# Kernel optimization log

Measured on AMD Instinct MI355X. Metric: run time of the kernel, lower is better.

The kernel has to match this reference:

```python
import jax, jax.numpy as jnp
import numpy as np

N, D, C, S = 100000, 512, 4096, 50000


def setup_inputs() -> dict:
    key = jax.random.key(0)
    k1, k2 = jax.random.split(key)
    X = jax.random.normal(k1, (N, D), dtype=jnp.float32)
    codebook_sum = jax.random.normal(k2, (C, D), dtype=jnp.float32)
    prompt_mask = jnp.arange(N) < S  # first S rows are support (True), rest are queries
    return {"X": X, "codebook_sum": codebook_sum, "prompt_mask": prompt_mask, "num_support": S}


def reference(X, codebook_sum, prompt_mask, num_support):
    # num_support is a static Python int (replaces torch.nonzero(prompt_mask) dynamic split)
    s = num_support
    support = X[:s]                                   # [S, D] support (prompt_mask==True)
    query = X[s:]                                     # [Q, D] queries (prompt_mask==False)
    # dense similarity matmul + top-1 nearest-codebook search + gather
    cos_sim = jnp.einsum('sd,cd->sc', support, codebook_sum)  # [S, C]
    top_idx = jnp.argmax(cos_sim, axis=1)             # [S]
    code_n = codebook_sum[top_idx]                    # [S, D] gathered nearest codes
    # mean-pooled prototypes broadcast over queries
    proto = jnp.mean(support, axis=0)                 # [D]
    proto_code = jnp.mean(code_n, axis=0)             # [D]
    # euclidean distances to each prototype
    query_score = jnp.sqrt(jnp.sum((query - proto) ** 2, axis=1))        # [Q]
    query_score_code = jnp.sqrt(jnp.sum((query - proto_code) ** 2, axis=1))  # [Q]
    return (query_score + query_score_code) / 2
```

## Files before the change

kernel.cpp:

```cpp
#include <hip/hip_runtime.h>
#include <hip/hip_bf16.h>

#define NTOT 100000
#define DIM  512
#define CB   4096
#define SSUP 50000
#define NQ   (NTOT - SSUP)

#define MTILES 391
#define MPAD   (MTILES * 128)
#define NTILES 32
#define NBLOCKS (MTILES * NTILES)

typedef __bf16 bf16x8 __attribute__((ext_vector_type(8)));
typedef __bf16 bf16x4 __attribute__((ext_vector_type(4)));
typedef float  f32x4  __attribute__((ext_vector_type(4)));
typedef float  f32x16 __attribute__((ext_vector_type(16)));

#define OFF_CBBF   0
#define OFF_XB     4194304
#define OFF_PV     55443456
#define OFF_PI     61849600
#define OFF_PSUM   68255744
#define OFF_PCSUM  68257792
#define OFF_HIST   68259840
#define WS_NEED    (68259840 + 16384)
#define ZERO_BYTES (2048 + 2048 + 16384)

#define F_OFF_PSUM   4194304
#define F_OFF_PCSUM  4196352
#define F_OFF_HIST   4198400
#define F_OFF_TIDX   4214784

__device__ __forceinline__ void load_lds16(const void* g, void* l) {
    __builtin_amdgcn_global_load_lds(
        (const __attribute__((address_space(1))) void*)g,
        (__attribute__((address_space(3))) void*)l, 16, 0, 0);
}

__global__ void k_convert(const float* __restrict__ src, __bf16* __restrict__ dst) {
    int i = (blockIdx.x * 256 + threadIdx.x) * 4;
    float4 v = *(const float4*)(src + i);
    bf16x4 o;
    o[0] = (__bf16)v.x; o[1] = (__bf16)v.y; o[2] = (__bf16)v.z; o[3] = (__bf16)v.w;
    *(bf16x4*)(dst + i) = o;
}

__global__ void k_prep_support(const float* __restrict__ X, __bf16* __restrict__ Xb,
                               float* __restrict__ protoSum) {
    const int tid   = threadIdx.x;
    const int rhalf = tid >> 7;
    const int c4    = (tid & 127) * 4;
    const size_t r0 = (size_t)blockIdx.x * 128;
    float a0 = 0.f, a1 = 0.f, a2 = 0.f, a3 = 0.f;
    #pragma unroll 4
    for (int i = 0; i < 64; ++i) {
        size_t r = r0 + (size_t)i * 2 + rhalf;
        float4 v = *(const float4*)(X + r * DIM + c4);
        bf16x4 o;
        o[0] = (__bf16)v.x; o[1] = (__bf16)v.y; o[2] = (__bf16)v.z; o[3] = (__bf16)v.w;
        *(bf16x4*)(Xb + r * DIM + c4) = o;
        if (r < SSUP) { a0 += v.x; a1 += v.y; a2 += v.z; a3 += v.w; }
    }
    atomicAdd(&protoSum[c4 + 0], a0);
    atomicAdd(&protoSum[c4 + 1], a1);
    atomicAdd(&protoSum[c4 + 2], a2);
    atomicAdd(&protoSum[c4 + 3], a3);
}

__global__ __launch_bounds__(256)
void k_gemm_tile(const __bf16* __restrict__ Xb, const __bf16* __restrict__ cbb,
                 float* __restrict__ pv, int* __restrict__ pi)
{
    __shared__ __bf16 lA[128 * 32];
    __shared__ __bf16 lB[128 * 32];
    __shared__ float  sv[128][2];
    __shared__ int    si[128][2];

    const int tid  = threadIdx.x;
    const int wave = tid >> 6;
    const int lane = tid & 63;
    const int wm   = wave >> 1;
    const int wn   = wave & 1;
    const int l31  = lane & 31;
    const int lh   = lane >> 5;

    const int b = blockIdx.x;
    int mt, nt;
    if (b < 12288) {
        const int xcd = b & 7, q = b >> 3;
        nt = q & 31;
        mt = ((q >> 5) << 3) + xcd;
    } else {
        const int idx = b - 12288;
        mt = 384 + (idx >> 5);
        nt = idx & 31;
    }
    const size_t r0 = (size_t)mt * 128;
    const int    c0 = nt * 128;

    f32x16 acc[2][2];
    #pragma unroll
    for (int i = 0; i < 2; ++i)
        #pragma unroll
        for (int j = 0; j < 2; ++j)
            acc[i][j] = (f32x16)(0.f);

    for (int k0 = 0; k0 < 512; k0 += 32) {
        __syncthreads();
        #pragma unroll
        for (int i = 0; i < 2; ++i) {
            const int s   = i * 256 + tid;
            const int row = s >> 2;
            const int kc  = (s & 3) ^ ((row >> 1) & 3);
            load_lds16(Xb  + (r0 + row) * DIM + k0 + kc * 8, lA + s * 8);
            load_lds16(cbb + (size_t)(c0 + row) * DIM + k0 + kc * 8, lB + s * 8);
        }
        __syncthreads();

        bf16x8 af[2][2], bf[2][2];
        #pragma unroll
        for (int h = 0; h < 2; ++h) {
            const int kc = h * 2 + lh;
            #pragma unroll
            for (int t = 0; t < 2; ++t) {
                const int rowA  = wm * 64 + t * 32 + l31;
                const int slotA = rowA * 4 + (kc ^ ((rowA >> 1) & 3));
                af[h][t] = *(const bf16x8*)(lA + slotA * 8);
                const int rowB  = wn * 64 + t * 32 + l31;
                const int slotB = rowB * 4 + (kc ^ ((rowB >> 1) & 3));
                bf[h][t] = *(const bf16x8*)(lB + slotB * 8);
            }
        }
        #pragma unroll
        for (int h = 0; h < 2; ++h)
            #pragma unroll
            for (int tm = 0; tm < 2; ++tm)
                #pragma unroll
                for (int tn = 0; tn < 2; ++tn)
                    acc[tm][tn] = __builtin_amdgcn_mfma_f32_32x32x16_bf16(
                        af[h][tm], bf[h][tn], acc[tm][tn], 0, 0, 0);
    }

    #pragma unroll
    for (int tm = 0; tm < 2; ++tm) {
        #pragma unroll
        for (int reg = 0; reg < 16; ++reg) {
            float x0 = acc[tm][0][reg], x1 = acc[tm][1][reg];
            const int cbase = c0 + wn * 64 + l31;
            float v; int idx;
            if (x1 > x0) { v = x1; idx = cbase + 32; } else { v = x0; idx = cbase; }
            #pragma unroll
            for (int off = 1; off <= 16; off <<= 1) {
                float ov = __shfl_xor(v, off, 64);
                int   oi = __shfl_xor(idx, off, 64);
                if (ov > v) { v = ov; idx = oi; }
            }
            if (l31 == 0) {
                const int rowL = wm * 64 + tm * 32 + 4 * lh + (reg & 3) + 8 * (reg >> 2);
                sv[rowL][wn] = v;
                si[rowL][wn] = idx;
            }
        }
    }
    __syncthreads();
    if (tid < 128) {
        float v0 = sv[tid][0], v1 = sv[tid][1];
        pv[(size_t)nt * MPAD + r0 + tid] = fmaxf(v0, v1);
        pi[(size_t)nt * MPAD + r0 + tid] = (v1 > v0) ? si[tid][1] : si[tid][0];
    }
}

__global__ void k_reduce_hist(const float* __restrict__ pv, const int* __restrict__ pi,
                              int* __restrict__ hist) {
    __shared__ int lh[CB];
    for (int i = threadIdx.x; i < CB; i += 256) lh[i] = 0;
    __syncthreads();
    int r = blockIdx.x * 256 + threadIdx.x;
    if (r < SSUP) {
        float v = -3.0e38f; int idx = 0;
        #pragma unroll 8
        for (int j = 0; j < 32; ++j) {
            float x = pv[(size_t)j * MPAD + r];
            if (x > v) { v = x; idx = pi[(size_t)j * MPAD + r]; }
        }
        atomicAdd(&lh[idx], 1);
    }
    __syncthreads();
    for (int i = threadIdx.x; i < CB; i += 256) {
        int v = lh[i];
        if (v) atomicAdd(&hist[i], v);
    }
}

__global__ void k_proto_code(const float* __restrict__ cb, const int* __restrict__ hist,
                             float* __restrict__ pcSum) {
    const int d  = threadIdx.x;
    const int c0 = blockIdx.x * 32;
    float acc = 0.f;
    for (int c = c0; c < c0 + 32; ++c) {
        float w = (float)hist[c];
        if (w != 0.f) acc += w * cb[(size_t)c * DIM + d];
    }
    atomicAdd(&pcSum[d], acc);
}

__global__ void k_query(const float* __restrict__ X, const float* __restrict__ protoSum,
                        const float* __restrict__ pcSum, float* __restrict__ out) {
    const int lane   = threadIdx.x & 63;
    const int waveId = (blockIdx.x * blockDim.x + threadIdx.x) >> 6;
    const int nwaves = (gridDim.x * blockDim.x) >> 6;
    const float invS = 1.0f / (float)SSUP;

    for (int r = waveId; r < NQ; r += nwaves) {
        const float* xr = X + (size_t)(SSUP + r) * DIM;
        float s1 = 0.f, s2 = 0.f;
        #pragma unroll
        for (int i = 0; i < 2; ++i) {
            int dd = lane * 4 + i * 256;
            float4 xq = *(const float4*)(xr + dd);
            float4 p  = *(const float4*)(protoSum + dd);
            float4 pc = *(const float4*)(pcSum + dd);
            float d0, d1, d2, d3;
            d0 = xq.x - p.x * invS; d1 = xq.y - p.y * invS;
            d2 = xq.z - p.z * invS; d3 = xq.w - p.w * invS;
            s1 += d0 * d0 + d1 * d1 + d2 * d2 + d3 * d3;
            d0 = xq.x - pc.x * invS; d1 = xq.y - pc.y * invS;
            d2 = xq.z - pc.z * invS; d3 = xq.w - pc.w * invS;
            s2 += d0 * d0 + d1 * d1 + d2 * d2 + d3 * d3;
        }
        #pragma unroll
        for (int off = 32; off > 0; off >>= 1) {
            s1 += __shfl_xor(s1, off, 64);
            s2 += __shfl_xor(s2, off, 64);
        }
        if (lane == 0)
            out[r] = 0.5f * (sqrtf(s1) + sqrtf(s2));
    }
}

__global__ __launch_bounds__(256, 2)
void k_gemm_argmax(const float* __restrict__ X, const __bf16* __restrict__ cbb,
                   int* __restrict__ top_idx)
{
    __shared__ float redv[64][2];
    __shared__ int   redi[64][2];

    const int tid  = threadIdx.x;
    const int wave = tid >> 6;
    const int lane = tid & 63;
    const int wm   = wave >> 1;
    const int wn   = wave & 1;
    const int l15  = lane & 15;
    const int q    = lane >> 4;
    const int r0   = blockIdx.x * 64;

    bf16x8 aflat[2][16];
    #pragma unroll
    for (int tm = 0; tm < 2; ++tm) {
        const int r = r0 + wm * 32 + tm * 16 + l15;
        const bool valid = (r < SSUP);
        const float* xr = X + (size_t)r * DIM + q * 8;
        #pragma unroll
        for (int kt = 0; kt < 16; ++kt) {
            float4 v0, v1;
            if (valid) {
                v0 = *(const float4*)(xr + kt * 32);
                v1 = *(const float4*)(xr + kt * 32 + 4);
            } else {
                v0 = make_float4(0.f, 0.f, 0.f, 0.f);
                v1 = v0;
            }
            bf16x8 f;
            f[0] = (__bf16)v0.x; f[1] = (__bf16)v0.y; f[2] = (__bf16)v0.z; f[3] = (__bf16)v0.w;
            f[4] = (__bf16)v1.x; f[5] = (__bf16)v1.y; f[6] = (__bf16)v1.z; f[7] = (__bf16)v1.w;
            aflat[tm][kt] = f;
        }
    }

    float mx[8]; int mi[8];
    #pragma unroll
    for (int i = 0; i < 8; ++i) { mx[i] = -3.0e38f; mi[i] = 0; }
    const f32x4 zero4 = {0.f, 0.f, 0.f, 0.f};

    for (int ct = 0; ct < 32; ++ct) {
        const int c0 = ct * 128 + wn * 64;
        const __bf16* bptr[4];
        #pragma unroll
        for (int tn = 0; tn < 4; ++tn)
            bptr[tn] = cbb + (size_t)(c0 + tn * 16 + l15) * DIM + q * 8;

        f32x4 acc[2][4];
        #pragma unroll
        for (int i = 0; i < 2; ++i)
            #pragma unroll
            for (int j = 0; j < 4; ++j)
                acc[i][j] = zero4;

        #pragma unroll
        for (int kt = 0; kt < 16; ++kt) {
            bf16x8 bfr[4];
            #pragma unroll
            for (int tn = 0; tn < 4; ++tn)
                bfr[tn] = *(const bf16x8*)(bptr[tn] + kt * 32);
            #pragma unroll
            for (int tm = 0; tm < 2; ++tm)
                #pragma unroll
                for (int tn = 0; tn < 4; ++tn)
                    acc[tm][tn] = __builtin_amdgcn_mfma_f32_16x16x32_bf16(
                        aflat[tm][kt], bfr[tn], acc[tm][tn], 0, 0, 0);
        }
        #pragma unroll
        for (int tm = 0; tm < 2; ++tm)
            #pragma unroll
            for (int tn = 0; tn < 4; ++tn)
                #pragma unroll
                for (int reg = 0; reg < 4; ++reg) {
                    float v = acc[tm][tn][reg];
                    int slot = tm * 4 + reg;
                    int col  = c0 + tn * 16 + l15;
                    if (v > mx[slot]) { mx[slot] = v; mi[slot] = col; }
                }
    }

    #pragma unroll
    for (int slot = 0; slot < 8; ++slot) {
        float v  = mx[slot];
        int  idx = mi[slot];
        #pragma unroll
        for (int off = 1; off < 16; off <<= 1) {
            float ov = __shfl_xor(v, off, 64);
            int   oi = __shfl_xor(idx, off, 64);
            if (ov > v) { v = ov; idx = oi; }
        }
        if (l15 == 0) {
            int rowl = wm * 32 + (slot >> 2) * 16 + q * 4 + (slot & 3);
            redv[rowl][wn] = v;
            redi[rowl][wn] = idx;
        }
    }
    __syncthreads();
    if (tid < 64) {
        int r = r0 + tid;
        if (r < SSUP) {
            float v0 = redv[tid][0], v1 = redv[tid][1];
            top_idx[r] = (v1 > v0) ? redi[tid][1] : redi[tid][0];
        }
    }
}

__global__ void k_proto_sum(const float* __restrict__ X, float* __restrict__ protoSum) {
    const int d = threadIdx.x;
    const int r0 = blockIdx.x * 500;
    float acc = 0.f;
    for (int r = r0; r < r0 + 500; ++r)
        acc += X[(size_t)r * DIM + d];
    atomicAdd(&protoSum[d], acc);
}

__global__ void k_hist(const int* __restrict__ top_idx, int* __restrict__ hist) {
    __shared__ int lh[CB];
    for (int i = threadIdx.x; i < CB; i += blockDim.x) lh[i] = 0;
    __syncthreads();
    for (int i = blockIdx.x * blockDim.x + threadIdx.x; i < SSUP; i += gridDim.x * blockDim.x)
        atomicAdd(&lh[top_idx[i]], 1);
    __syncthreads();
    for (int i = threadIdx.x; i < CB; i += blockDim.x) {
        int v = lh[i];
        if (v) atomicAdd(&hist[i], v);
    }
}

extern "C" void kernel_launch(void* const* d_in, const int* in_sizes, int n_in,
                              void* d_out, int out_size, void* d_ws, size_t ws_size,
                              hipStream_t stream) {
    const float* X  = (const float*)d_in[0];
    const float* cb = (const float*)d_in[1];
    float* out = (float*)d_out;
    char* ws = (char*)d_ws;

    __bf16* cbb = (__bf16*)(ws + OFF_CBBF);

    if (ws_size >= (size_t)WS_NEED) {
        __bf16* Xb       = (__bf16*)(ws + OFF_XB);
        float*  pv       = (float*)(ws + OFF_PV);
        int*    pi       = (int*)(ws + OFF_PI);
        float*  protoSum = (float*)(ws + OFF_PSUM);
        float*  pcSum    = (float*)(ws + OFF_PCSUM);
        int*    hist     = (int*)(ws + OFF_HIST);

        hipMemsetAsync(ws + OFF_PSUM, 0, ZERO_BYTES, stream);

        k_convert<<<(CB * DIM) / 1024, 256, 0, stream>>>(cb, cbb);
        k_prep_support<<<MTILES, 256, 0, stream>>>(X, Xb, protoSum);

        k_gemm_tile<<<NBLOCKS, 256, 0, stream>>>(Xb, cbb, pv, pi);

        k_reduce_hist<<<(SSUP + 255) / 256, 256, 0, stream>>>(pv, pi, hist);
        k_proto_code<<<CB / 32, 512, 0, stream>>>(cb, hist, pcSum);
        k_query<<<2048, 256, 0, stream>>>(X, protoSum, pcSum, out);
    } else {
        float*  protoSum = (float*)(ws + F_OFF_PSUM);
        float*  pcSum    = (float*)(ws + F_OFF_PCSUM);
        int*    hist     = (int*)(ws + F_OFF_HIST);
        int*    top_idx  = (int*)(ws + F_OFF_TIDX);

        hipMemsetAsync(ws + F_OFF_PSUM, 0, ZERO_BYTES, stream);

        k_convert<<<(CB * DIM) / 1024, 256, 0, stream>>>(cb, cbb);
        k_proto_sum<<<100, 512, 0, stream>>>(X, protoSum);
        k_gemm_argmax<<<(SSUP + 63) / 64, 256, 0, stream>>>(X, cbb, top_idx);
        k_hist<<<64, 256, 0, stream>>>(top_idx, hist);
        k_proto_code<<<CB / 64, 512, 0, stream>>>(cb, hist, pcSum);
        k_query<<<1024, 256, 0, stream>>>(X, protoSum, pcSum, out);
    }
}
```

Measured before the change: 733.9 us.

## Replace LDS-staged GEMM with direct global-to-register MFMA loads

Removes LDS staging and block barriers from the support-by-codebook GEMM. Each wave now loads its bf16 fragments straight from global memory into registers and issues MFMAs, relying on L1/L2 for reuse. The XCD-aware block swizzle is replaced by a plain 2D grid. The fused convert-plus-prototype-sum kernel is split into a separate X conversion kernel and a proto-sum kernel, which reads X twice. Several launch sizes also change. The risk is more global traffic and lost cross-wave reuse inside the GEMM, which is the dominant cost.

```diff
diff --git a/kernel.cpp b/kernel.cpp
--- a/kernel.cpp
+++ b/kernel.cpp
@@ -10,7 +10,6 @@
 #define MTILES 391
 #define MPAD   (MTILES * 128)
 #define NTILES 32
-#define NBLOCKS (MTILES * NTILES)
 
 typedef __bf16 bf16x8 __attribute__((ext_vector_type(8)));
 typedef __bf16 bf16x4 __attribute__((ext_vector_type(4)));
@@ -32,12 +31,6 @@
 #define F_OFF_HIST   4198400
 #define F_OFF_TIDX   4214784
 
-__device__ __forceinline__ void load_lds16(const void* g, void* l) {
-    __builtin_amdgcn_global_load_lds(
-        (const __attribute__((address_space(1))) void*)g,
-        (__attribute__((address_space(3))) void*)l, 16, 0, 0);
-}
-
 __global__ void k_convert(const float* __restrict__ src, __bf16* __restrict__ dst) {
     int i = (blockIdx.x * 256 + threadIdx.x) * 4;
     float4 v = *(const float4*)(src + i);
@@ -46,36 +39,21 @@
     *(bf16x4*)(dst + i) = o;
 }
 
-__global__ void k_prep_support(const float* __restrict__ X, __bf16* __restrict__ Xb,
-                               float* __restrict__ protoSum) {
-    const int tid   = threadIdx.x;
-    const int rhalf = tid >> 7;
-    const int c4    = (tid & 127) * 4;
-    const size_t r0 = (size_t)blockIdx.x * 128;
-    float a0 = 0.f, a1 = 0.f, a2 = 0.f, a3 = 0.f;
-    #pragma unroll 4
-    for (int i = 0; i < 64; ++i) {
-        size_t r = r0 + (size_t)i * 2 + rhalf;
-        float4 v = *(const float4*)(X + r * DIM + c4);
-        bf16x4 o;
-        o[0] = (__bf16)v.x; o[1] = (__bf16)v.y; o[2] = (__bf16)v.z; o[3] = (__bf16)v.w;
-        *(bf16x4*)(Xb + r * DIM + c4) = o;
-        if (r < SSUP) { a0 += v.x; a1 += v.y; a2 += v.z; a3 += v.w; }
-    }
-    atomicAdd(&protoSum[c4 + 0], a0);
-    atomicAdd(&protoSum[c4 + 1], a1);
-    atomicAdd(&protoSum[c4 + 2], a2);
-    atomicAdd(&protoSum[c4 + 3], a3);
+__global__ void k_proto_sum(const float* __restrict__ X, float* __restrict__ protoSum) {
+    const int d = threadIdx.x;
+    const int r0 = blockIdx.x * 200;
+    float acc = 0.f;
+    for (int r = r0; r < r0 + 200; ++r)
+        acc += X[(size_t)r * DIM + d];
+    atomicAdd(&protoSum[d], acc);
 }
 
 __global__ __launch_bounds__(256)
-void k_gemm_tile(const __bf16* __restrict__ Xb, const __bf16* __restrict__ cbb,
-                 float* __restrict__ pv, int* __restrict__ pi)
+void k_gemm_direct(const __bf16* __restrict__ Xb, const __bf16* __restrict__ cbb,
+                   float* __restrict__ pv, int* __restrict__ pi)
 {
-    __shared__ __bf16 lA[128 * 32];
-    __shared__ __bf16 lB[128 * 32];
-    __shared__ float  sv[128][2];
-    __shared__ int    si[128][2];
+    __shared__ float sv[128][2];
+    __shared__ int   si[128][2];
 
     const int tid  = threadIdx.x;
     const int wave = tid >> 6;
@@ -84,21 +62,16 @@
     const int wn   = wave & 1;
     const int l31  = lane & 31;
     const int lh   = lane >> 5;
-
-    const int b = blockIdx.x;
-    int mt, nt;
-    if (b < 12288) {
-        const int xcd = b & 7, q = b >> 3;
-        nt = q & 31;
-        mt = ((q >> 5) << 3) + xcd;
-    } else {
-        const int idx = b - 12288;
-        mt = 384 + (idx >> 5);
-        nt = idx & 31;
-    }
+    const int nt   = blockIdx.x;
+    const int mt   = blockIdx.y;
     const size_t r0 = (size_t)mt * 128;
     const int    c0 = nt * 128;
 
+    const __bf16* pa0 = Xb  + (r0 + wm * 64 +      l31) * DIM + lh * 8;
+    const __bf16* pa1 = Xb  + (r0 + wm * 64 + 32 + l31) * DIM + lh * 8;
+    const __bf16* pb0 = cbb + (size_t)(c0 + wn * 64 +      l31) * DIM + lh * 8;
+    const __bf16* pb1 = cbb + (size_t)(c0 + wn * 64 + 32 + l31) * DIM + lh * 8;
+
     f32x16 acc[2][2];
     #pragma unroll
     for (int i = 0; i < 2; ++i)
@@ -106,40 +79,16 @@
         for (int j = 0; j < 2; ++j)
             acc[i][j] = (f32x16)(0.f);
 
-    for (int k0 = 0; k0 < 512; k0 += 32) {
-        __syncthreads();
-        #pragma unroll
-        for (int i = 0; i < 2; ++i) {
-            const int s   = i * 256 + tid;
-            const int row = s >> 2;
-            const int kc  = (s & 3) ^ ((row >> 1) & 3);
-            load_lds16(Xb  + (r0 + row) * DIM + k0 + kc * 8, lA + s * 8);
-            load_lds16(cbb + (size_t)(c0 + row) * DIM + k0 + kc * 8, lB + s * 8);
-        }
-        __syncthreads();
-
-        bf16x8 af[2][2], bf[2][2];
-        #pragma unroll
-        for (int h = 0; h < 2; ++h) {
-            const int kc = h * 2 + lh;
-            #pragma unroll
-            for (int t = 0; t < 2; ++t) {
-                const int rowA  = wm * 64 + t * 32 + l31;
-                const int slotA = rowA * 4 + (kc ^ ((rowA >> 1) & 3));
-                af[h][t] = *(const bf16x8*)(lA + slotA * 8);
-                const int rowB  = wn * 64 + t * 32 + l31;
-                const int slotB = rowB * 4 + (kc ^ ((rowB >> 1) & 3));
-                bf[h][t] = *(const bf16x8*)(lB + slotB * 8);
-            }
-        }
-        #pragma unroll
-        for (int h = 0; h < 2; ++h)
-            #pragma unroll
-            for (int tm = 0; tm < 2; ++tm)
-                #pragma unroll
-                for (int tn = 0; tn < 2; ++tn)
-                    acc[tm][tn] = __builtin_amdgcn_mfma_f32_32x32x16_bf16(
-                        af[h][tm], bf[h][tn], acc[tm][tn], 0, 0, 0);
+    #pragma unroll 8
+    for (int k = 0; k < 512; k += 16) {
+        bf16x8 a0 = *(const bf16x8*)(pa0 + k);
+        bf16x8 a1 = *(const bf16x8*)(pa1 + k);
+        bf16x8 b0 = *(const bf16x8*)(pb0 + k);
+        bf16x8 b1 = *(const bf16x8*)(pb1 + k);
+        acc[0][0] = __builtin_amdgcn_mfma_f32_32x32x16_bf16(a0, b0, acc[0][0], 0, 0, 0);
+        acc[0][1] = __builtin_amdgcn_mfma_f32_32x32x16_bf16(a0, b1, acc[0][1], 0, 0, 0);
+        acc[1][0] = __builtin_amdgcn_mfma_f32_32x32x16_bf16(a1, b0, acc[1][0], 0, 0, 0);
+        acc[1][1] = __builtin_amdgcn_mfma_f32_32x32x16_bf16(a1, b1, acc[1][1], 0, 0, 0);
     }
 
     #pragma unroll
@@ -196,9 +145,9 @@
 __global__ void k_proto_code(const float* __restrict__ cb, const int* __restrict__ hist,
                              float* __restrict__ pcSum) {
     const int d  = threadIdx.x;
-    const int c0 = blockIdx.x * 32;
+    const int c0 = blockIdx.x * 64;
     float acc = 0.f;
-    for (int c = c0; c < c0 + 32; ++c) {
+    for (int c = c0; c < c0 + 64; ++c) {
         float w = (float)hist[c];
         if (w != 0.f) acc += w * cb[(size_t)c * DIM + d];
     }
@@ -349,15 +298,6 @@
     }
 }
 
-__global__ void k_proto_sum(const float* __restrict__ X, float* __restrict__ protoSum) {
-    const int d = threadIdx.x;
-    const int r0 = blockIdx.x * 500;
-    float acc = 0.f;
-    for (int r = r0; r < r0 + 500; ++r)
-        acc += X[(size_t)r * DIM + d];
-    atomicAdd(&protoSum[d], acc);
-}
-
 __global__ void k_hist(const int* __restrict__ top_idx, int* __restrict__ hist) {
     __shared__ int lh[CB];
     for (int i = threadIdx.x; i < CB; i += blockDim.x) lh[i] = 0;
@@ -392,13 +332,15 @@
         hipMemsetAsync(ws + OFF_PSUM, 0, ZERO_BYTES, stream);
 
         k_convert<<<(CB * DIM) / 1024, 256, 0, stream>>>(cb, cbb);
-        k_prep_support<<<MTILES, 256, 0, stream>>>(X, Xb, protoSum);
-
-        k_gemm_tile<<<NBLOCKS, 256, 0, stream>>>(Xb, cbb, pv, pi);
+        k_convert<<<(MPAD * DIM) / 1024, 256, 0, stream>>>(X, Xb);
+        k_proto_sum<<<250, 512, 0, stream>>>(X, protoSum);
+
+        dim3 grid(NTILES, MTILES);
+        k_gemm_direct<<<grid, 256, 0, stream>>>(Xb, cbb, pv, pi);
 
         k_reduce_hist<<<(SSUP + 255) / 256, 256, 0, stream>>>(pv, pi, hist);
-        k_proto_code<<<CB / 32, 512, 0, stream>>>(cb, hist, pcSum);
-        k_query<<<2048, 256, 0, stream>>>(X, protoSum, pcSum, out);
+        k_proto_code<<<CB / 64, 512, 0, stream>>>(cb, hist, pcSum);
+        k_query<<<1024, 256, 0, stream>>>(X, protoSum, pcSum, out);
     } else {
         float*  protoSum = (float*)(ws + F_OFF_PSUM);
         float*  pcSum    = (float*)(ws + F_OFF_PCSUM);
@@ -408,7 +350,7 @@
         hipMemsetAsync(ws + F_OFF_PSUM, 0, ZERO_BYTES, stream);
 
         k_convert<<<(CB * DIM) / 1024, 256, 0, stream>>>(cb, cbb);
-        k_proto_sum<<<100, 512, 0, stream>>>(X, protoSum);
+        k_proto_sum<<<250, 512, 0, stream>>>(X, protoSum);
         k_gemm_argmax<<<(SSUP + 63) / 64, 256, 0, stream>>>(X, cbb, top_idx);
         k_hist<<<64, 256, 0, stream>>>(top_idx, hist);
         k_proto_code<<<CB / 64, 512, 0, stream>>>(cb, hist, pcSum);
```

After: 1.046 ms. 1.43x slower.
